# Kernel optimization log

Measured on AMD Instinct MI355X. Metric: run time of the kernel, lower is better.

Reference implementation:

```python
import jax, jax.numpy as jnp
import numpy as np

NB_TF = 4          # brightness, contrast, invert-blend, gain
MAGS_PER_TF = 9    # magnitudes 0.1 .. 0.9 (range(1, int(mag*10)) with mag=1)
NB_OP = NB_TF * MAGS_PER_TF


def setup_inputs() -> dict:
    key = jax.random.key(0)
    k1, k2, k3 = jax.random.split(key, 3)
    B, C, H, W = 256, 3, 224, 224
    x = jax.random.uniform(k1, (B, C, H, W), dtype=jnp.float32)
    # per-image sampled op index (Categorical over a uniform distribution)
    sample = jax.random.randint(k2, (B,), 0, NB_OP)
    # per-op Bernoulli(prob=0.5) coin: 1 -> apply the op, 0 -> identity
    apply_mask = jax.random.randint(k3, (NB_OP,), 0, 2).astype(jnp.int32)
    return {"x": x, "sample": sample, "apply_mask": apply_mask}


def _apply_ops(x, sample, apply_mask):
    # Decode op index -> (tf type, magnitude). op_list layout: for tf in TFs:
    #   for m in 1..9: (tf, prob, m/10)
    tf_idx = sample // MAGS_PER_TF                       # [B]
    mag = ((sample % MAGS_PER_TF) + 1).astype(x.dtype) / 10.0
    mag = mag[:, None, None, None]                       # [B,1,1,1]

    mean = jnp.mean(x, axis=(1, 2, 3), keepdims=True)    # per-image mean
    t_bright = jnp.clip(x + mag, 0.0, 1.0)               # brightness shift
    t_contr = jnp.clip(mean + (x - mean) * (1.0 + mag), 0.0, 1.0)
    t_inv = (1.0 - mag) * x + mag * (1.0 - x)            # blend with inverted
    t_gain = jnp.clip(x * (1.0 + mag), 0.0, 1.0)         # multiplicative gain

    stack = jnp.stack([t_bright, t_contr, t_inv, t_gain], axis=1)  # [B,4,C,H,W]
    sel = tf_idx[:, None, None, None, None]              # [B,1,1,1,1]
    transformed = jnp.take_along_axis(stack, sel, axis=1)[:, 0]    # [B,C,H,W]

    applied = (apply_mask[sample] > 0)[:, None, None, None]
    return jnp.where(applied, transformed, x)


def reference(x, sample, apply_mask):
    # N_seqTF = 1 -> single round of sample -> gather -> transform -> scatter,
    # here expressed as a fully vectorized per-image select.
    return _apply_ops(x, sample, apply_mask)
```

## Files before the change

### kernel.cpp

```cpp
#include <hip/hip_runtime.h>

#define N_IMG   256
#define HW      (224 * 224)
#define CHW     (3 * HW)
#define V4      (CHW / 4)
#define THREADS 256

#define CHUNKS      21
#define CHUNK_V4    (V4 / CHUNKS)
#define PER_THREAD  (CHUNK_V4 / THREADS)

#define MAGS_PER_TF 9

typedef float fvec4 __attribute__((ext_vector_type(4)));

__device__ __forceinline__ float clip01(float v) {
    return fminf(fmaxf(v, 0.0f), 1.0f);
}

__global__ __launch_bounds__(THREADS) void mean_kernel(
        const float* __restrict__ x,
        const int* __restrict__ sample,
        const int* __restrict__ apply_mask,
        float* __restrict__ partials ) {
    const int img  = blockIdx.y;
    const int part = blockIdx.x;
    const int s    = sample[img];
    if ((s / MAGS_PER_TF) != 1 || apply_mask[s] <= 0) return;

    const fvec4* xp = (const fvec4*)x + (size_t)img * V4 + (size_t)part * CHUNK_V4;
    fvec4 v[PER_THREAD];
#pragma unroll
    for (int k = 0; k < PER_THREAD; ++k)
        v[k] = xp[threadIdx.x + k * THREADS];

    float sum = 0.0f;
#pragma unroll
    for (int k = 0; k < PER_THREAD; ++k)
        sum += (v[k].x + v[k].y) + (v[k].z + v[k].w);

#pragma unroll
    for (int off = 32; off > 0; off >>= 1)
        sum += __shfl_down(sum, off, 64);

    __shared__ float wsum[THREADS / 64];
    if ((threadIdx.x & 63) == 0) wsum[threadIdx.x >> 6] = sum;
    __syncthreads();
    if (threadIdx.x == 0) {
        float t = (wsum[0] + wsum[1]) + (wsum[2] + wsum[3]);
        partials[img * CHUNKS + part] = t;
    }
}

__global__ __launch_bounds__(THREADS) void apply_kernel(
        const float* __restrict__ x,
        const int* __restrict__ sample,
        const int* __restrict__ apply_mask,
        const float* __restrict__ partials,
        float* __restrict__ out) {
    const int img   = blockIdx.y;
    const int chunk = blockIdx.x;
    const int s     = sample[img];
    const int tf    = s / MAGS_PER_TF;
    const float mag = (float)(s % MAGS_PER_TF + 1) / 10.0f;
    const bool applied = apply_mask[s] > 0;

    const size_t base = (size_t)img * V4 + (size_t)chunk * CHUNK_V4 + threadIdx.x;
    const fvec4* xp = (const fvec4*)x + base;
    fvec4*       op = (fvec4*)out + base;

    fvec4 v[PER_THREAD];
#pragma unroll
    for (int k = 0; k < PER_THREAD; ++k)
        v[k] = xp[k * THREADS];

    fvec4 r[PER_THREAD];

    if (!applied) {
#pragma unroll
        for (int k = 0; k < PER_THREAD; ++k) r[k] = v[k];
    } else if (tf == 0) {
#pragma unroll
        for (int k = 0; k < PER_THREAD; ++k) {
            r[k].x = clip01(v[k].x + mag);
            r[k].y = clip01(v[k].y + mag);
            r[k].z = clip01(v[k].z + mag);
            r[k].w = clip01(v[k].w + mag);
        }
    } else if (tf == 1) {
        float mean = 0.0f;
#pragma unroll
        for (int p = 0; p < CHUNKS; ++p) mean += partials[img * CHUNKS + p];
        mean /= (float)CHW;
        const float g = 1.0f + mag;
#pragma unroll
        for (int k = 0; k < PER_THREAD; ++k) {
            r[k].x = clip01(mean + (v[k].x - mean) * g);
            r[k].y = clip01(mean + (v[k].y - mean) * g);
            r[k].z = clip01(mean + (v[k].z - mean) * g);
            r[k].w = clip01(mean + (v[k].w - mean) * g);
        }
    } else if (tf == 2) {
        const float a = 1.0f - mag;
#pragma unroll
        for (int k = 0; k < PER_THREAD; ++k) {
            r[k].x = a * v[k].x + mag * (1.0f - v[k].x);
            r[k].y = a * v[k].y + mag * (1.0f - v[k].y);
            r[k].z = a * v[k].z + mag * (1.0f - v[k].z);
            r[k].w = a * v[k].w + mag * (1.0f - v[k].w);
        }
    } else {
        const float g = 1.0f + mag;
#pragma unroll
        for (int k = 0; k < PER_THREAD; ++k) {
            r[k].x = clip01(v[k].x * g);
            r[k].y = clip01(v[k].y * g);
            r[k].z = clip01(v[k].z * g);
            r[k].w = clip01(v[k].w * g);
        }
    }

#pragma unroll
    for (int k = 0; k < PER_THREAD; ++k)
        __builtin_nontemporal_store(r[k], op + k * THREADS);
}

extern "C" void kernel_launch(void* const* d_in, const int* in_sizes, int n_in,
                              void* d_out, int out_size, void* d_ws, size_t ws_size,
                              hipStream_t stream) {
    const float* x          = (const float*)d_in[0];
    const int*   sample     = (const int*)d_in[1];
    const int*   apply_mask = (const int*)d_in[2];
    float*       out        = (float*)d_out;
    float*       partials   = (float*)d_ws;

    dim3 mgrid(CHUNKS, N_IMG);
    mean_kernel<<<mgrid, THREADS, 0, stream>>>(x, sample, apply_mask, partials);

    dim3 agrid(CHUNKS, N_IMG);
    apply_kernel<<<agrid, THREADS, 0, stream>>>(x, sample, apply_mask, partials, out);
}
```

Baseline: 274.7 us.

## Fuse mean and apply kernels, recomputing per-image mean within each block

Replaces the two-kernel scheme (partial-sum kernel plus apply kernel) with a single fused kernel. Each block of a contrast image recomputes the whole-image mean itself, so there is no second launch and no partials round-trip. Chunks drop from 21 to 7, and each block handles three groups of seven vec4 loads. The invert-blend is simplified algebraically to a*x+mag. The cost is redundant reads: for contrast images each of the 7 blocks reads the full image to get the mean, and there are fewer, larger blocks.

```diff
diff --git a/kernel.cpp b/kernel.cpp
--- a/kernel.cpp
+++ b/kernel.cpp
@@ -6,9 +6,11 @@
 #define V4      (CHW / 4)
 #define THREADS 256
 
-#define CHUNKS      21
+#define CHUNKS      7
 #define CHUNK_V4    (V4 / CHUNKS)
 #define PER_THREAD  (CHUNK_V4 / THREADS)
+#define GROUPS      3
+#define GSIZE       7
 
 #define MAGS_PER_TF 9
 
@@ -18,111 +20,90 @@
     return fminf(fmaxf(v, 0.0f), 1.0f);
 }
 
-__global__ __launch_bounds__(THREADS) void mean_kernel(
+__global__ __launch_bounds__(THREADS) void fused_kernel(
         const float* __restrict__ x,
         const int* __restrict__ sample,
         const int* __restrict__ apply_mask,
-        float* __restrict__ partials ) {
-    const int img  = blockIdx.y;
-    const int part = blockIdx.x;
-    const int s    = sample[img];
-    if ((s / MAGS_PER_TF) != 1 || apply_mask[s] <= 0) return;
-
-    const fvec4* xp = (const fvec4*)x + (size_t)img * V4 + (size_t)part * CHUNK_V4;
-    fvec4 v[PER_THREAD];
-#pragma unroll
-    for (int k = 0; k < PER_THREAD; ++k)
-        v[k] = xp[threadIdx.x + k * THREADS];
-
-    float sum = 0.0f;
-#pragma unroll
-    for (int k = 0; k < PER_THREAD; ++k)
-        sum += (v[k].x + v[k].y) + (v[k].z + v[k].w);
-
-#pragma unroll
-    for (int off = 32; off > 0; off >>= 1)
-        sum += __shfl_down(sum, off, 64);
-
-    __shared__ float wsum[THREADS / 64];
-    if ((threadIdx.x & 63) == 0) wsum[threadIdx.x >> 6] = sum;
-    __syncthreads();
-    if (threadIdx.x == 0) {
-        float t = (wsum[0] + wsum[1]) + (wsum[2] + wsum[3]);
-        partials[img * CHUNKS + part] = t;
-    }
-}
-
-__global__ __launch_bounds__(THREADS) void apply_kernel(
-        const float* __restrict__ x,
-        const int* __restrict__ sample,
-        const int* __restrict__ apply_mask,
-        const float* __restrict__ partials,
         float* __restrict__ out) {
     const int img   = blockIdx.y;
     const int chunk = blockIdx.x;
     const int s     = sample[img];
     const int tf    = s / MAGS_PER_TF;
-    const float mag = (float)(s % MAGS_PER_TF + 1) / 10.0f;
+    const float mag = (float)(s % MAGS_PER_TF + 1) * 0.1f;
     const bool applied = apply_mask[s] > 0;
 
-    const size_t base = (size_t)img * V4 + (size_t)chunk * CHUNK_V4 + threadIdx.x;
-    const fvec4* xp = (const fvec4*)x + base;
-    fvec4*       op = (fvec4*)out + base;
+    const fvec4* ximg = (const fvec4*)x + (size_t)img * V4;
 
-    fvec4 v[PER_THREAD];
+    float mean = 0.0f;
+    if (applied && tf == 1) {
+        float sum = 0.0f;
+#pragma unroll 7
+        for (int k = 0; k < V4 / THREADS; ++k) {
+            fvec4 t = ximg[threadIdx.x + k * THREADS];
+            sum += (t.x + t.y) + (t.z + t.w);
+        }
 #pragma unroll
-    for (int k = 0; k < PER_THREAD; ++k)
-        v[k] = xp[k * THREADS];
-
-    fvec4 r[PER_THREAD];
-
-    if (!applied) {
-#pragma unroll
-        for (int k = 0; k < PER_THREAD; ++k) r[k] = v[k];
-    } else if (tf == 0) {
-#pragma unroll
-        for (int k = 0; k < PER_THREAD; ++k) {
-            r[k].x = clip01(v[k].x + mag);
-            r[k].y = clip01(v[k].y + mag);
-            r[k].z = clip01(v[k].z + mag);
-            r[k].w = clip01(v[k].w + mag);
-        }
-    } else if (tf == 1) {
-        float mean = 0.0f;
-#pragma unroll
-        for (int p = 0; p < CHUNKS; ++p) mean += partials[img * CHUNKS + p];
-        mean /= (float)CHW;
-        const float g = 1.0f + mag;
-#pragma unroll
-        for (int k = 0; k < PER_THREAD; ++k) {
-            r[k].x = clip01(mean + (v[k].x - mean) * g);
-            r[k].y = clip01(mean + (v[k].y - mean) * g);
-            r[k].z = clip01(mean + (v[k].z - mean) * g);
-            r[k].w = clip01(mean + (v[k].w - mean) * g);
-        }
-    } else if (tf == 2) {
-        const float a = 1.0f - mag;
-#pragma unroll
-        for (int k = 0; k < PER_THREAD; ++k) {
-            r[k].x = a * v[k].x + mag * (1.0f - v[k].x);
-            r[k].y = a * v[k].y + mag * (1.0f - v[k].y);
-            r[k].z = a * v[k].z + mag * (1.0f - v[k].z);
-            r[k].w = a * v[k].w + mag * (1.0f - v[k].w);
-        }
-    } else {
-        const float g = 1.0f + mag;
-#pragma unroll
-        for (int k = 0; k < PER_THREAD; ++k) {
-            r[k].x = clip01(v[k].x * g);
-            r[k].y = clip01(v[k].y * g);
-            r[k].z = clip01(v[k].z * g);
-            r[k].w = clip01(v[k].w * g);
-        }
+        for (int off = 32; off > 0; off >>= 1)
+            sum += __shfl_down(sum, off, 64);
+        __shared__ float wsum[THREADS / 64];
+        if ((threadIdx.x & 63) == 0) wsum[threadIdx.x >> 6] = sum;
+        __syncthreads();
+        mean = ((wsum[0] + wsum[1]) + (wsum[2] + wsum[3])) * (1.0f / (float)CHW);
     }
 
+    const size_t base = (size_t)chunk * CHUNK_V4 + threadIdx.x;
+    const fvec4* xp = ximg + base;
+    fvec4*       op = (fvec4*)out + (size_t)img * V4 + base;
+
+    const float g1 = 1.0f + mag;
+    const float a2 = 1.0f - 2.0f * mag;
+
 #pragma unroll
-    for (int k = 0; k < PER_THREAD; ++k)
-        __builtin_nontemporal_store(r[k], op + k * THREADS);
+    for (int g = 0; g < GROUPS; ++g) {
+        fvec4 v[GSIZE];
+#pragma unroll
+        for (int k = 0; k < GSIZE; ++k)
+            v[k] = xp[(g * GSIZE + k) * THREADS];
+
+        if (!applied) {
+        } else if (tf == 0) {
+#pragma unroll
+            for (int k = 0; k < GSIZE; ++k) {
+                v[k].x = clip01(v[k].x + mag);
+                v[k].y = clip01(v[k].y + mag);
+                v[k].z = clip01(v[k].z + mag);
+                v[k].w = clip01(v[k].w + mag);
+            }
+        } else if (tf == 1) {
+#pragma unroll
+            for (int k = 0; k < GSIZE; ++k) {
+                v[k].x = clip01(mean + (v[k].x - mean) * g1);
+                v[k].y = clip01(mean + (v[k].y - mean) * g1);
+                v[k].z = clip01(mean + (v[k].z - mean) * g1);
+                v[k].w = clip01(mean + (v[k].w - mean) * g1);
+            }
+        } else if (tf == 2) {
+#pragma unroll
+            for (int k = 0; k < GSIZE; ++k) {
+                v[k].x = a2 * v[k].x + mag;
+                v[k].y = a2 * v[k].y + mag;
+                v[k].z = a2 * v[k].z + mag;
+                v[k].w = a2 * v[k].w + mag;
+            }
+        } else {
+#pragma unroll
+            for (int k = 0; k < GSIZE; ++k) {
+                v[k].x = clip01(v[k].x * g1);
+                v[k].y = clip01(v[k].y * g1);
+                v[k].z = clip01(v[k].z * g1);
+                v[k].w = clip01(v[k].w * g1);
+            }
+        }
+
+#pragma unroll
+        for (int k = 0; k < GSIZE; ++k)
+            __builtin_nontemporal_store(v[k], op + (g * GSIZE + k) * THREADS);
+    }
 }
 
 extern "C" void kernel_launch(void* const* d_in, const int* in_sizes, int n_in,
@@ -132,11 +113,7 @@
     const int*   sample     = (const int*)d_in[1];
     const int*   apply_mask = (const int*)d_in[2];
     float*       out        = (float*)d_out;
-    float*       partials   = (float*)d_ws;
 
-    dim3 mgrid(CHUNKS, N_IMG);
-    mean_kernel<<<mgrid, THREADS, 0, stream>>>(x, sample, apply_mask, partials);
-
-    dim3 agrid(CHUNKS, N_IMG);
-    apply_kernel<<<agrid, THREADS, 0, stream>>>(x, sample, apply_mask, partials, out);
+    dim3 grid(CHUNKS, N_IMG);
+    fused_kernel<<<grid, THREADS, 0, stream>>>(x, sample, apply_mask, out);
 }
```

After: 283.6 us. 3.3% more time.
